# Kernel tuning notes

Measured on AMD Instinct MI355X. Metric: run time of the kernel, lower is better.

Reference implementation:

```python
import jax, jax.numpy as jnp
import numpy as np

N_NODES = 100000
HID = 128
N_LAYERS = 3
N_EDGES = 1600000
EPS = 1e-5


def setup_inputs() -> dict:
    key = jax.random.key(0)
    ks = jax.random.split(key, 10)
    H, L = HID, N_LAYERS
    # edge_index: row 0 = src, row 1 = dst (PyG source_to_target flow)
    edge_index = jax.random.randint(ks[0], (2, N_EDGES), 0, N_NODES, dtype=jnp.int32)
    # xavier-uniform embedding
    lim = float(np.sqrt(6.0 / (N_NODES + H)))
    emb = jax.random.uniform(ks[1], (N_NODES, H), jnp.float32, -lim, lim)
    s = 1.0 / np.sqrt(H)
    Wl = jax.random.uniform(ks[2], (L, H, H), jnp.float32, -s, s)  # lin_l (neighbors), has bias
    bl = jax.random.uniform(ks[3], (L, H), jnp.float32, -s, s)
    Wr = jax.random.uniform(ks[4], (L, H, H), jnp.float32, -s, s)  # lin_r (root), no bias
    ln_gamma = jnp.ones((L, H), jnp.float32)
    ln_beta = jnp.zeros((L, H), jnp.float32)
    sj = 1.0 / np.sqrt(H * (L + 1))
    jkW = jax.random.uniform(ks[5], (H, H * (L + 1)), jnp.float32, -sj, sj)
    jkb = jax.random.uniform(ks[6], (H,), jnp.float32, -sj, sj)
    return {"emb": emb, "Wl": Wl, "bl": bl, "Wr": Wr,
            "ln_gamma": ln_gamma, "ln_beta": ln_beta,
            "jkW": jkW, "jkb": jkb, "edge_index": edge_index}


def _layernorm(x, gamma, beta):
    mu = jnp.mean(x, axis=-1, keepdims=True)
    var = jnp.mean(jnp.square(x - mu), axis=-1, keepdims=True)
    return (x - mu) * jax.lax.rsqrt(var + EPS) * gamma + beta


def reference(emb, Wl, bl, Wr, ln_gamma, ln_beta, jkW, jkb, edge_index):
    src, dst = edge_index[0], edge_index[1]
    n = emb.shape[0]
    # in-degree for mean aggregation (clamped to avoid div-by-zero)
    deg = jax.ops.segment_sum(jnp.ones_like(dst, dtype=emb.dtype), dst, num_segments=n)
    inv_deg = (1.0 / jnp.maximum(deg, 1.0))[:, None]
    x = emb
    xs = [x]
    for i in range(N_LAYERS):
        x_prev = x
        # scatter-mean of neighbor features (gather [E,H] -> segment_sum [N,H])
        agg = jax.ops.segment_sum(x[src], dst, num_segments=n) * inv_deg
        # SAGEConv: lin_l(agg) + lin_r(x)
        x = agg @ Wl[i].T + bl[i] + x @ Wr[i].T
        x = _layernorm(x, ln_gamma[i], ln_beta[i])
        x = jax.nn.relu(x)
        # dropout is identity in eval mode
        if i > 0:
            x = x + x_prev
        xs.append(x)
    # jumping-knowledge concat + projection
    x = jnp.concatenate(xs, axis=1) @ jkW.T + jkb
    return x
```

## Files before the change

kernel.cpp:

```cpp
#include <hip/hip_runtime.h>
#include <hip/hip_bf16.h>
#include <stdint.h>

#define HID 128
#define BSHIFT 7
#define NBLK 64

typedef __attribute__((ext_vector_type(8))) __bf16 bf16x8;
typedef __attribute__((ext_vector_type(4))) float f32x4;

static __device__ __forceinline__ float bf2f(ushort h){
  union { uint u; float f; } c; c.u = ((uint)h) << 16; return c.f;
}
static __device__ __forceinline__ ushort f2bf(float f){
  union { float f; uint u; } c; c.f = f;
  uint u = c.u;
  return (ushort)((u + 0x7fffu + ((u >> 16) & 1u)) >> 16);
}
static __device__ __forceinline__ bf16x8 load8(const ushort* p){
  return *(const bf16x8*)p;
}

__global__ void k_cvt(const float* __restrict__ in, ushort* __restrict__ out, int n){
  int i = blockIdx.x * 256 + threadIdx.x;
  if (i < n) out[i] = f2bf(in[i]);
}

__global__ void k_cvtw(const float* __restrict__ Wl, const float* __restrict__ Wr,
                       ushort* __restrict__ outF, int total){
  int o = blockIdx.x * 256 + threadIdx.x;
  if (o >= total) return;
  int layer = o >> 15;
  int r = o & 32767;
  int e    = r & 7;
  int lane = (r >> 3) & 63;
  int jt   = (r >> 9) & 7;
  int mat  = (r >> 12) & 1;
  int kt   = r >> 13;
  int l16 = lane & 15, quad = lane >> 4;
  int j = l16 * 8 + jt;
  int k = kt * 32 + quad * 8 + e;
  const float* W = mat ? Wr : Wl;
  outF[o] = f2bf(W[layer * 16384 + j * 128 + k]);
}

__global__ void k_cvtjk(const float* __restrict__ jkW, ushort* __restrict__ outF){
  int o = blockIdx.x * 256 + threadIdx.x;
  int e    = o & 7;
  int lane = (o >> 3) & 63;
  int jt   = (o >> 9) & 7;
  int kt   = o >> 12;
  int l16 = lane & 15, quad = lane >> 4;
  int j = l16 * 4 + (jt & 3) + (jt >> 2) * 64;
  int k = kt * 32 + quad * 8 + e;
  outF[o] = f2bf(jkW[j * 512 + k]);
}

__global__ __launch_bounds__(1024) void k_count(
    const int* __restrict__ dst, int* __restrict__ rowcnt, int E, int NB, int es){
  __shared__ int h[1024];
  int blk = blockIdx.x;
  for (int i = threadIdx.x; i < NB; i += 1024) h[i] = 0;
  __syncthreads();
  int e0 = blk * es, e1 = min(e0 + es, E);
  for (int e = e0 + threadIdx.x; e < e1; e += 1024)
    atomicAdd(&h[dst[e] >> BSHIFT], 1);
  __syncthreads();
  for (int i = threadIdx.x; i < NB; i += 1024)
    rowcnt[blk * NB + i] = h[i];
}

__global__ __launch_bounds__(1024) void k_colscan(
    int* __restrict__ rowcnt, int* __restrict__ bbase, int NB, int nblk){
  int b = threadIdx.x;
  int total = 0;
  if (b < NB)
    for (int r = 0; r < nblk; r++) total += rowcnt[r * NB + b];
  int lane = b & 63, w = b >> 6;
  int x = total;
  #pragma unroll
  for (int d = 1; d < 64; d <<= 1){ int y = __shfl_up(x, d, 64); if (lane >= d) x += y; }
  __shared__ int tmp[16];
  if (lane == 63) tmp[w] = x;
  __syncthreads();
  if (b < 64){
    int s = (lane < 16) ? tmp[lane] : 0;
    #pragma unroll
    for (int d = 1; d < 16; d <<= 1){ int y = __shfl_up(s, d, 64); if (lane >= d) s += y; }
    if (lane < 16) tmp[lane] = s;
  }
  __syncthreads();
  int base = ((w > 0) ? tmp[w - 1] : 0) + x - total;
  if (b < NB){
    bbase[b] = base;
    int acc = base;
    for (int r = 0; r < nblk; r++){
      int v = rowcnt[r * NB + b];
      rowcnt[r * NB + b] = acc;
      acc += v;
    }
    if (b == NB - 1) bbase[NB] = acc;
  }
}

__global__ __launch_bounds__(1024) void k_place(
    const int* __restrict__ src, const int* __restrict__ dst,
    const int* __restrict__ rowcnt, uint* __restrict__ binned, int E, int NB, int es){
  __shared__ int cur[1024];
  int blk = blockIdx.x;
  for (int i = threadIdx.x; i < NB; i += 1024) cur[i] = rowcnt[blk * NB + i];
  __syncthreads();
  int e0 = blk * es, e1 = min(e0 + es, E);
  for (int e = e0 + threadIdx.x; e < e1; e += 1024){
    int d = dst[e];
    int b = d >> BSHIFT;
    int pos = atomicAdd(&cur[b], 1);
    binned[pos] = ((uint)src[e] << BSHIFT) | (uint)(d & 127);
  }
}

__global__ __launch_bounds__(256) void k_bpass(
    const uint* __restrict__ binned, const int* __restrict__ bbase,
    int* __restrict__ csr, int* __restrict__ offs, int* __restrict__ cnt, int N){
  int b = blockIdx.x;
  int n0 = b << BSHIFT;
  int tid = threadIdx.x;
  __shared__ int lcnt[128], loffs[128];
  if (tid < 128) lcnt[tid] = 0;
  __syncthreads();
  int base = bbase[b];
  int m = bbase[b + 1] - base;
  const uint* bp = binned + base;
  uint vv[12]; int slot[12];
  #pragma unroll
  for (int u = 0; u < 12; u++){
    int i = tid + u * 256;
    if (i < m){
      uint v = bp[i];
      vv[u] = v;
      slot[u] = atomicAdd(&lcnt[v & 127], 1);
    }
  }
  __syncthreads();
  if (tid < 64){
    int a0 = lcnt[tid * 2], a1 = lcnt[tid * 2 + 1];
    int s = a0 + a1;
    int x = s;
    #pragma unroll
    for (int d = 1; d < 64; d <<= 1){ int y = __shfl_up(x, d, 64); if (tid >= d) x += y; }
    int excl = x - s;
    loffs[tid * 2] = excl;
    loffs[tid * 2 + 1] = excl + a0;
  }
  __syncthreads();
  if (tid < 128 && n0 + tid < N){
    cnt[n0 + tid] = lcnt[tid];
    offs[n0 + tid] = base + loffs[tid];
  }
  #pragma unroll
  for (int u = 0; u < 12; u++){
    int i = tid + u * 256;
    if (i < m){
      uint v = vv[u];
      csr[base + loffs[v & 127] + slot[u]] = (int)(v >> BSHIFT);
    }
  }
}

__global__ __launch_bounds__(256) void k_aggregate(
    const ushort* __restrict__ x, const int* __restrict__ csr,
    const int* __restrict__ offs, const int* __restrict__ cnt,
    ushort* __restrict__ agg, int N){
  int node = blockIdx.x * 4 + (threadIdx.x >> 6);
  int lane = threadIdx.x & 63;
  if (node >= N) return;
  int half = lane >> 5;
  int l32  = lane & 31;
  int beg = offs[node], d = cnt[node];
  if (d == 0){
    if (half == 0){
      uint2 z = {0u, 0u};
      *(uint2*)(agg + (size_t)node * HID + l32 * 4) = z;
    }
    return;
  }
  const int* __restrict__ cp = csr + beg;
  float s0 = 0.f, s1 = 0.f, s2 = 0.f, s3 = 0.f;
  int i = 0;
  for (; i + 16 <= d; i += 16){
    int idx[8];
    #pragma unroll
    for (int u = 0; u < 8; u++) idx[u] = cp[i + 2 * u + half];
    uint2 v[8];
    #pragma unroll
    for (int u = 0; u < 8; u++)
      v[u] = *(const uint2*)(x + (size_t)idx[u] * HID + l32 * 4);
    #pragma unroll
    for (int u = 0; u < 8; u++){
      s0 += bf2f((ushort)v[u].x);
      s1 += bf2f((ushort)(v[u].x >> 16));
      s2 += bf2f((ushort)v[u].y);
      s3 += bf2f((ushort)(v[u].y >> 16));
    }
  }
  if (i < d){
    int idx[8]; float w[8];
    #pragma unroll
    for (int u = 0; u < 8; u++){
      int pos = i + 2 * u + half;
      bool ok = pos < d;
      pos = ok ? pos : d - 1;
      idx[u] = cp[pos];
      w[u] = ok ? 1.f : 0.f;
    }
    uint2 v[8];
    #pragma unroll
    for (int u = 0; u < 8; u++)
      v[u] = *(const uint2*)(x + (size_t)idx[u] * HID + l32 * 4);
    #pragma unroll
    for (int u = 0; u < 8; u++){
      s0 = fmaf(w[u], bf2f((ushort)v[u].x), s0);
      s1 = fmaf(w[u], bf2f((ushort)(v[u].x >> 16)), s1);
      s2 = fmaf(w[u], bf2f((ushort)v[u].y), s2);
      s3 = fmaf(w[u], bf2f((ushort)(v[u].y >> 16)), s3);
    }
  }
  s0 += __shfl_xor(s0, 32, 64);
  s1 += __shfl_xor(s1, 32, 64);
  s2 += __shfl_xor(s2, 32, 64);
  s3 += __shfl_xor(s3, 32, 64);
  if (half == 0){
    float inv = 1.0f / fmaxf((float)d, 1.0f);
    uint2 o;
    o.x = (uint)f2bf(s0 * inv) | ((uint)f2bf(s1 * inv) << 16);
    o.y = (uint)f2bf(s2 * inv) | ((uint)f2bf(s3 * inv) << 16);
    *(uint2*)(agg + (size_t)node * HID + l32 * 4) = o;
  }
}

template<int HAS_RES>
__global__ __launch_bounds__(256, 3) void k_layer(
    const ushort* __restrict__ agg, const ushort* __restrict__ xin,
    const ushort* __restrict__ Wf,
    const float* __restrict__ bl, const float* __restrict__ gamma,
    const float* __restrict__ beta,
    ushort* __restrict__ xout, int N){
  int tid = threadIdx.x;
  int wv = tid >> 6, lane = tid & 63;
  int quad = lane >> 4, l16 = lane & 15;
  int rowbase = blockIdx.x * 128 + wv * 32;
  int r0 = rowbase + l16;      if (r0 >= N) r0 = N - 1;
  int r1 = rowbase + 16 + l16; if (r1 >= N) r1 = N - 1;

  bf16x8 aL0[4], aL1[4], aR0[4], aR1[4];
  #pragma unroll
  for (int kt = 0; kt < 4; kt++){
    int ao = kt * 32 + quad * 8;
    aL0[kt] = load8(agg + (size_t)r0 * HID + ao);
    aL1[kt] = load8(agg + (size_t)r1 * HID + ao);
    aR0[kt] = load8(xin + (size_t)r0 * HID + ao);
    aR1[kt] = load8(xin + (size_t)r1 * HID + ao);
  }

  float4 bi0 = *(const float4*)(bl + l16 * 8);
  float4 bi1 = *(const float4*)(bl + l16 * 8 + 4);
  float4 g0 = *(const float4*)(gamma + l16 * 8);
  float4 g1 = *(const float4*)(gamma + l16 * 8 + 4);
  float4 be0 = *(const float4*)(beta + l16 * 8);
  float4 be1 = *(const float4*)(beta + l16 * 8 + 4);
  float gg[8] = {g0.x, g0.y, g0.z, g0.w, g1.x, g1.y, g1.z, g1.w};
  float bb[8] = {be0.x, be0.y, be0.z, be0.w, be1.x, be1.y, be1.z, be1.w};
  float bia[8] = {bi0.x, bi0.y, bi0.z, bi0.w, bi1.x, bi1.y, bi1.z, bi1.w};

  f32x4 acc[2][8];
  #pragma unroll
  for (int jt = 0; jt < 8; jt++){
    float b = bia[jt];
    f32x4 c = {b, b, b, b};
    acc[0][jt] = c; acc[1][jt] = c;
  }

  #pragma unroll
  for (int kt = 0; kt < 4; kt++){
    #pragma unroll
    for (int jt = 0; jt < 8; jt++){
      bf16x8 bL = load8(Wf + ((kt * 16 + jt) * 64 + lane) * 8);
      bf16x8 bR = load8(Wf + ((kt * 16 + 8 + jt) * 64 + lane) * 8);
      acc[0][jt] = __builtin_amdgcn_mfma_f32_16x16x32_bf16(aL0[kt], bL, acc[0][jt], 0, 0, 0);
      acc[1][jt] = __builtin_amdgcn_mfma_f32_16x16x32_bf16(aL1[kt], bL, acc[1][jt], 0, 0, 0);
      acc[0][jt] = __builtin_amdgcn_mfma_f32_16x16x32_bf16(aR0[kt], bR, acc[0][jt], 0, 0, 0);
      acc[1][jt] = __builtin_amdgcn_mfma_f32_16x16x32_bf16(aR1[kt], bR, acc[1][jt], 0, 0, 0);
    }
  }

  #pragma unroll
  for (int rt = 0; rt < 2; rt++){
    float s1[4] = {0,0,0,0}, s2[4] = {0,0,0,0};
    #pragma unroll
    for (int jt = 0; jt < 8; jt++){
      #pragma unroll
      for (int r = 0; r < 4; r++){ float v = acc[rt][jt][r]; s1[r] += v; s2[r] += v * v; }
    }
    #pragma unroll
    for (int m = 1; m < 16; m <<= 1){
      #pragma unroll
      for (int r = 0; r < 4; r++){
        s1[r] += __shfl_xor(s1[r], m, 64);
        s2[r] += __shfl_xor(s2[r], m, 64);
      }
    }
    #pragma unroll
    for (int r = 0; r < 4; r++){
      float mu = s1[r] * (1.f / 128.f);
      float var = s2[r] * (1.f / 128.f) - mu * mu;
      float rs = rsqrtf(var + 1e-5f);
      int row = rowbase + rt * 16 + quad * 4 + r;
      int rowc = row < N ? row : N - 1;
      uint rw[4] = {0u, 0u, 0u, 0u};
      if (HAS_RES){
        uint4 rv = *(const uint4*)(xin + (size_t)rowc * HID + l16 * 8);
        rw[0] = rv.x; rw[1] = rv.y; rw[2] = rv.z; rw[3] = rv.w;
      }
      uint ow[4];
      #pragma unroll
      for (int p = 0; p < 4; p++){
        float v0 = (acc[rt][2 * p][r] - mu) * rs * gg[2 * p] + bb[2 * p];
        float v1 = (acc[rt][2 * p + 1][r] - mu) * rs * gg[2 * p + 1] + bb[2 * p + 1];
        v0 = fmaxf(v0, 0.f);
        v1 = fmaxf(v1, 0.f);
        if (HAS_RES){
          v0 += bf2f((ushort)(rw[p] & 0xffffu));
          v1 += bf2f((ushort)(rw[p] >> 16));
        }
        ow[p] = (uint)f2bf(v0) | ((uint)f2bf(v1) << 16);
      }
      uint4 o;
      o.x = ow[0]; o.y = ow[1]; o.z = ow[2]; o.w = ow[3];
      if (row < N)
        *(uint4*)(xout + (size_t)row * HID + l16 * 8) = o;
    }
  }
}

__global__ __launch_bounds__(256, 3) void k_jk(
    const ushort* __restrict__ emb, const ushort* __restrict__ x1,
    const ushort* __restrict__ x2, const ushort* __restrict__ x3,
    const ushort* __restrict__ Wf,
    const float* __restrict__ jkb, float* __restrict__ out, int N){
  int tid = threadIdx.x;
  int wv = tid >> 6, lane = tid & 63;
  int quad = lane >> 4, l16 = lane & 15;
  int rowbase = blockIdx.x * 128 + wv * 32;
  int r0 = rowbase + l16;      if (r0 >= N) r0 = N - 1;
  int r1 = rowbase + 16 + l16; if (r1 >= N) r1 = N - 1;

  float4 jb0 = *(const float4*)(jkb + l16 * 4);
  float4 jb1 = *(const float4*)(jkb + 64 + l16 * 4);
  float bia[8] = {jb0.x, jb0.y, jb0.z, jb0.w, jb1.x, jb1.y, jb1.z, jb1.w};

  f32x4 acc[2][8];
  #pragma unroll
  for (int jt = 0; jt < 8; jt++){
    float b = bia[jt];
    f32x4 c = {b, b, b, b};
    acc[0][jt] = c; acc[1][jt] = c;
  }

  const ushort* srcs[4] = {emb, x1, x2, x3};
  #pragma unroll
  for (int s = 0; s < 4; s++){
    const ushort* sp = srcs[s];
    bf16x8 a0[4], a1[4];
    #pragma unroll
    for (int kt = 0; kt < 4; kt++){
      int ao = kt * 32 + quad * 8;
      a0[kt] = load8(sp + (size_t)r0 * HID + ao);
      a1[kt] = load8(sp + (size_t)r1 * HID + ao);
    }
    #pragma unroll
    for (int kt = 0; kt < 4; kt++){
      int ktg = s * 4 + kt;
      #pragma unroll
      for (int jt = 0; jt < 8; jt++){
        bf16x8 bW = load8(Wf + ((ktg * 8 + jt) * 64 + lane) * 8);
        acc[0][jt] = __builtin_amdgcn_mfma_f32_16x16x32_bf16(a0[kt], bW, acc[0][jt], 0, 0, 0);
        acc[1][jt] = __builtin_amdgcn_mfma_f32_16x16x32_bf16(a1[kt], bW, acc[1][jt], 0, 0, 0);
      }
    }
  }

  #pragma unroll
  for (int rt = 0; rt < 2; rt++){
    #pragma unroll
    for (int r = 0; r < 4; r++){
      int row = rowbase + rt * 16 + quad * 4 + r;
      if (row < N){
        f32x4 v0 = {acc[rt][0][r], acc[rt][1][r], acc[rt][2][r], acc[rt][3][r]};
        f32x4 v1 = {acc[rt][4][r], acc[rt][5][r], acc[rt][6][r], acc[rt][7][r]};
        *(f32x4*)(out + (size_t)row * HID + l16 * 4) = v0;
        *(f32x4*)(out + (size_t)row * HID + 64 + l16 * 4) = v1;
      }
    }
  }
}

extern "C" void kernel_launch(void* const* d_in, const int* in_sizes, int n_in,
                              void* d_out, int out_size, void* d_ws, size_t ws_size,
                              hipStream_t stream){
  const float* emb   = (const float*)d_in[0];
  const float* Wl    = (const float*)d_in[1];
  const float* bl    = (const float*)d_in[2];
  const float* Wr    = (const float*)d_in[3];
  const float* gamma = (const float*)d_in[4];
  const float* beta  = (const float*)d_in[5];
  const float* jkW   = (const float*)d_in[6];
  const float* jkb   = (const float*)d_in[7];
  const int*   eidx  = (const int*)d_in[8];
  int N = in_sizes[0] / HID;
  int E = in_sizes[8] / 2;
  const int* src = eidx;
  const int* dst = eidx + E;
  float* out = (float*)d_out;

  int NB = (N + 127) >> BSHIFT;
  int es = (E + NBLK - 1) / NBLK;

  char* w = (char*)d_ws;
  auto carve = [&](size_t bytes) -> char* {
    char* p = w; w += (bytes + 255) & ~(size_t)255; return p;
  };
  int Npad = ((N + 127) / 128) * 128;
  int* rowcnt   = (int*)carve((size_t)NBLK * NB * 4);
  int* bbase    = (int*)carve((size_t)(NB + 1) * 4);
  uint* binned  = (uint*)carve((size_t)E * 4);
  int* cnt      = (int*)carve((size_t)N * 4);
  int* offs     = (int*)carve((size_t)N * 4);
  int* csr      = (int*)carve((size_t)E * 4);
  ushort* Wfrag = (ushort*)carve((size_t)3 * 32768 * 2);
  ushort* jkWf  = (ushort*)carve((size_t)65536 * 2);
  ushort* embbf = (ushort*)carve((size_t)Npad * HID * 2);
  ushort* agg   = (ushort*)carve((size_t)Npad * HID * 2);
  ushort* x1    = (ushort*)carve((size_t)Npad * HID * 2);
  ushort* x2    = (ushort*)carve((size_t)Npad * HID * 2);
  ushort* x3    = (ushort*)carve((size_t)Npad * HID * 2);

  int nEmb = N * HID;
  k_cvtw<<<(3 * 32768 + 255) / 256, 256, 0, stream>>>(Wl, Wr, Wfrag, 3 * 32768);
  k_cvtjk<<<65536 / 256, 256, 0, stream>>>(jkW, jkWf);
  k_cvt<<<(nEmb + 255) / 256, 256, 0, stream>>>(emb, embbf, nEmb);

  k_count<<<NBLK, 1024, 0, stream>>>(dst, rowcnt, E, NB, es);
  k_colscan<<<1, 1024, 0, stream>>>(rowcnt, bbase, NB, NBLK);
  k_place<<<NBLK, 1024, 0, stream>>>(src, dst, rowcnt, binned, E, NB, es);
  k_bpass<<<NB, 256, 0, stream>>>(binned, bbase, csr, offs, cnt, N);

  int aggBlocks = (N + 3) / 4;
  int gemmBlocks = (N + 127) / 128;

  k_aggregate<<<aggBlocks, 256, 0, stream>>>(embbf, csr, offs, cnt, agg, N);
  k_layer<0><<<gemmBlocks, 256, 0, stream>>>(agg, embbf, Wfrag, bl, gamma, beta, x1, N);
  k_aggregate<<<aggBlocks, 256, 0, stream>>>(x1, csr, offs, cnt, agg, N);
  k_layer<1><<<gemmBlocks, 256, 0, stream>>>(agg, x1, Wfrag + 32768, bl + HID,
                                             gamma + HID, beta + HID, x2, N);
  k_aggregate<<<aggBlocks, 256, 0, stream>>>(x2, csr, offs, cnt, agg, N);
  k_layer<1><<<gemmBlocks, 256, 0, stream>>>(agg, x2, Wfrag + 2 * 32768, bl + 2 * HID,
                                             gamma + 2 * HID, beta + 2 * HID, x3, N);
  k_jk<<<gemmBlocks, 256, 0, stream>>>(embbf, x1, x2, x3, jkWf, jkb, out, N);
}
```

Measured before the change: 542.4 us.

## Cut register pressure in GEMM kernels and simplify gather address math

```diff
diff --git a/kernel.cpp b/kernel.cpp
--- a/kernel.cpp
+++ b/kernel.cpp
@@ -8,9 +8,13 @@
 
 typedef __attribute__((ext_vector_type(8))) __bf16 bf16x8;
 typedef __attribute__((ext_vector_type(4))) float f32x4;
+typedef __attribute__((ext_vector_type(2))) float f32x2;
 
 static __device__ __forceinline__ float bf2f(ushort h){
   union { uint u; float f; } c; c.u = ((uint)h) << 16; return c.f;
+}
+static __device__ __forceinline__ float u2f(uint u){
+  union { uint u; float f; } c; c.u = u; return c.f;
 }
 static __device__ __forceinline__ ushort f2bf(float f){
   union { float f; uint u; } c; c.f = f;
@@ -176,6 +180,7 @@
   if (node >= N) return;
   int half = lane >> 5;
   int l32  = lane & 31;
+  uint lb  = (uint)(l32 << 3);
   int beg = offs[node], d = cnt[node];
   if (d == 0){
     if (half == 0){
@@ -185,61 +190,61 @@
     return;
   }
   const int* __restrict__ cp = csr + beg;
-  float s0 = 0.f, s1 = 0.f, s2 = 0.f, s3 = 0.f;
+  const char* __restrict__ xb = (const char*)x;
+  f32x2 sx = {0.f, 0.f}, sy = {0.f, 0.f};
   int i = 0;
   for (; i + 16 <= d; i += 16){
-    int idx[8];
-    #pragma unroll
-    for (int u = 0; u < 8; u++) idx[u] = cp[i + 2 * u + half];
+    uint off[8];
+    #pragma unroll
+    for (int u = 0; u < 8; u++)
+      off[u] = ((uint)cp[i + 2 * u + half] << 8) + lb;
     uint2 v[8];
     #pragma unroll
     for (int u = 0; u < 8; u++)
-      v[u] = *(const uint2*)(x + (size_t)idx[u] * HID + l32 * 4);
+      v[u] = *(const uint2*)(xb + off[u]);
     #pragma unroll
     for (int u = 0; u < 8; u++){
-      s0 += bf2f((ushort)v[u].x);
-      s1 += bf2f((ushort)(v[u].x >> 16));
-      s2 += bf2f((ushort)v[u].y);
-      s3 += bf2f((ushort)(v[u].y >> 16));
+      f32x2 tx = { u2f(v[u].x << 16), u2f(v[u].x & 0xffff0000u) };
+      f32x2 ty = { u2f(v[u].y << 16), u2f(v[u].y & 0xffff0000u) };
+      sx += tx; sy += ty;
     }
   }
   if (i < d){
-    int idx[8]; float w[8];
+    uint off[8]; bool ok[8];
     #pragma unroll
     for (int u = 0; u < 8; u++){
       int pos = i + 2 * u + half;
-      bool ok = pos < d;
-      pos = ok ? pos : d - 1;
-      idx[u] = cp[pos];
-      w[u] = ok ? 1.f : 0.f;
+      ok[u] = pos < d;
+      off[u] = ((uint)cp[ok[u] ? pos : d - 1] << 8) + lb;
     }
     uint2 v[8];
     #pragma unroll
     for (int u = 0; u < 8; u++)
-      v[u] = *(const uint2*)(x + (size_t)idx[u] * HID + l32 * 4);
+      v[u] = *(const uint2*)(xb + off[u]);
     #pragma unroll
     for (int u = 0; u < 8; u++){
-      s0 = fmaf(w[u], bf2f((ushort)v[u].x), s0);
-      s1 = fmaf(w[u], bf2f((ushort)(v[u].x >> 16)), s1);
-      s2 = fmaf(w[u], bf2f((ushort)v[u].y), s2);
-      s3 = fmaf(w[u], bf2f((ushort)(v[u].y >> 16)), s3);
-    }
-  }
-  s0 += __shfl_xor(s0, 32, 64);
-  s1 += __shfl_xor(s1, 32, 64);
-  s2 += __shfl_xor(s2, 32, 64);
-  s3 += __shfl_xor(s3, 32, 64);
+      uint ax = ok[u] ? v[u].x : 0u;
+      uint ay = ok[u] ? v[u].y : 0u;
+      f32x2 tx = { u2f(ax << 16), u2f(ax & 0xffff0000u) };
+      f32x2 ty = { u2f(ay << 16), u2f(ay & 0xffff0000u) };
+      sx += tx; sy += ty;
+    }
+  }
+  sx.x += __shfl_xor(sx.x, 32, 64);
+  sx.y += __shfl_xor(sx.y, 32, 64);
+  sy.x += __shfl_xor(sy.x, 32, 64);
+  sy.y += __shfl_xor(sy.y, 32, 64);
   if (half == 0){
     float inv = 1.0f / fmaxf((float)d, 1.0f);
     uint2 o;
-    o.x = (uint)f2bf(s0 * inv) | ((uint)f2bf(s1 * inv) << 16);
-    o.y = (uint)f2bf(s2 * inv) | ((uint)f2bf(s3 * inv) << 16);
+    o.x = (uint)f2bf(sx.x * inv) | ((uint)f2bf(sx.y * inv) << 16);
+    o.y = (uint)f2bf(sy.x * inv) | ((uint)f2bf(sy.y * inv) << 16);
     *(uint2*)(agg + (size_t)node * HID + l32 * 4) = o;
   }
 }
 
 template<int HAS_RES>
-__global__ __launch_bounds__(256, 3) void k_layer(
+__global__ __launch_bounds__(256, 4) void k_layer(
     const ushort* __restrict__ agg, const ushort* __restrict__ xin,
     const ushort* __restrict__ Wf,
     const float* __restrict__ bl, const float* __restrict__ gamma,
@@ -251,47 +256,54 @@
   int rowbase = blockIdx.x * 128 + wv * 32;
   int r0 = rowbase + l16;      if (r0 >= N) r0 = N - 1;
   int r1 = rowbase + 16 + l16; if (r1 >= N) r1 = N - 1;
-
-  bf16x8 aL0[4], aL1[4], aR0[4], aR1[4];
+  int aq = quad * 8;
+
+  const ushort* pa0 = agg + (size_t)r0 * HID;
+  const ushort* pa1 = agg + (size_t)r1 * HID;
+  const ushort* px0 = xin + (size_t)r0 * HID;
+  const ushort* px1 = xin + (size_t)r1 * HID;
+
+  f32x4 acc[2][8];
+  {
+    float4 bi0 = *(const float4*)(bl + l16 * 8);
+    float4 bi1 = *(const float4*)(bl + l16 * 8 + 4);
+    float bia[8] = {bi0.x, bi0.y, bi0.z, bi0.w, bi1.x, bi1.y, bi1.z, bi1.w};
+    #pragma unroll
+    for (int jt = 0; jt < 8; jt++){
+      float b = bia[jt];
+      f32x4 c = {b, b, b, b};
+      acc[0][jt] = c; acc[1][jt] = c;
+    }
+  }
+
+  bf16x8 c0 = load8(pa0 + aq), c1 = load8(pa1 + aq);
+  bf16x8 c2 = load8(px0 + aq), c3 = load8(px1 + aq);
   #pragma unroll
   for (int kt = 0; kt < 4; kt++){
-    int ao = kt * 32 + quad * 8;
-    aL0[kt] = load8(agg + (size_t)r0 * HID + ao);
-    aL1[kt] = load8(agg + (size_t)r1 * HID + ao);
-    aR0[kt] = load8(xin + (size_t)r0 * HID + ao);
-    aR1[kt] = load8(xin + (size_t)r1 * HID + ao);
-  }
-
-  float4 bi0 = *(const float4*)(bl + l16 * 8);
-  float4 bi1 = *(const float4*)(bl + l16 * 8 + 4);
+    bf16x8 n0 = c0, n1 = c1, n2 = c2, n3 = c3;
+    if (kt < 3){
+      int ao = (kt + 1) * 32 + aq;
+      n0 = load8(pa0 + ao); n1 = load8(pa1 + ao);
+      n2 = load8(px0 + ao); n3 = load8(px1 + ao);
+    }
+    #pragma unroll
+    for (int jt = 0; jt < 8; jt++){
+      bf16x8 bL = load8(Wf + ((kt * 16 + jt) * 64 + lane) * 8);
+      bf16x8 bR = load8(Wf + ((kt * 16 + 8 + jt) * 64 + lane) * 8);
+      acc[0][jt] = __builtin_amdgcn_mfma_f32_16x16x32_bf16(c0, bL, acc[0][jt], 0, 0, 0);
+      acc[1][jt] = __builtin_amdgcn_mfma_f32_16x16x32_bf16(c1, bL, acc[1][jt], 0, 0, 0);
+      acc[0][jt] = __builtin_amdgcn_mfma_f32_16x16x32_bf16(c2, bR, acc[0][jt], 0, 0, 0);
+      acc[1][jt] = __builtin_amdgcn_mfma_f32_16x16x32_bf16(c3, bR, acc[1][jt], 0, 0, 0);
+    }
+    c0 = n0; c1 = n1; c2 = n2; c3 = n3;
+  }
+
   float4 g0 = *(const float4*)(gamma + l16 * 8);
   float4 g1 = *(const float4*)(gamma + l16 * 8 + 4);
   float4 be0 = *(const float4*)(beta + l16 * 8);
   float4 be1 = *(const float4*)(beta + l16 * 8 + 4);
   float gg[8] = {g0.x, g0.y, g0.z, g0.w, g1.x, g1.y, g1.z, g1.w};
   float bb[8] = {be0.x, be0.y, be0.z, be0.w, be1.x, be1.y, be1.z, be1.w};
-  float bia[8] = {bi0.x, bi0.y, bi0.z, bi0.w, bi1.x, bi1.y, bi1.z, bi1.w};
-
-  f32x4 acc[2][8];
-  #pragma unroll
-  for (int jt = 0; jt < 8; jt++){
-    float b = bia[jt];
-    f32x4 c = {b, b, b, b};
-    acc[0][jt] = c; acc[1][jt] = c;
-  }
-
-  #pragma unroll
-  for (int kt = 0; kt < 4; kt++){
-    #pragma unroll
-    for (int jt = 0; jt < 8; jt++){
-      bf16x8 bL = load8(Wf + ((kt * 16 + jt) * 64 + lane) * 8);
-      bf16x8 bR = load8(Wf + ((kt * 16 + 8 + jt) * 64 + lane) * 8);
-      acc[0][jt] = __builtin_amdgcn_mfma_f32_16x16x32_bf16(aL0[kt], bL, acc[0][jt], 0, 0, 0);
-      acc[1][jt] = __builtin_amdgcn_mfma_f32_16x16x32_bf16(aL1[kt], bL, acc[1][jt], 0, 0, 0);
-      acc[0][jt] = __builtin_amdgcn_mfma_f32_16x16x32_bf16(aR0[kt], bR, acc[0][jt], 0, 0, 0);
-      acc[1][jt] = __builtin_amdgcn_mfma_f32_16x16x32_bf16(aR1[kt], bR, acc[1][jt], 0, 0, 0);
-    }
-  }
 
   #pragma unroll
   for (int rt = 0; rt < 2; rt++){
@@ -342,7 +354,7 @@
   }
 }
 
-__global__ __launch_bounds__(256, 3) void k_jk(
+__global__ __launch_bounds__(256, 4) void k_jk(
     const ushort* __restrict__ emb, const ushort* __restrict__ x1,
     const ushort* __restrict__ x2, const ushort* __restrict__ x3,
     const ushort* __restrict__ Wf,
@@ -353,50 +365,51 @@
   int rowbase = blockIdx.x * 128 + wv * 32;
   int r0 = rowbase + l16;      if (r0 >= N) r0 = N - 1;
   int r1 = rowbase + 16 + l16; if (r1 >= N) r1 = N - 1;
+  int aq = quad * 8;
+  size_t o0 = (size_t)r0 * HID, o1 = (size_t)r1 * HID;
+
+  f32x4 acc[2][8];
+  #pragma unroll
+  for (int jt = 0; jt < 8; jt++){
+    f32x4 z = {0.f, 0.f, 0.f, 0.f};
+    acc[0][jt] = z; acc[1][jt] = z;
+  }
+
+  const ushort* srcs[4] = {emb, x1, x2, x3};
+  bf16x8 a0 = load8(emb + o0 + aq);
+  bf16x8 a1 = load8(emb + o1 + aq);
+  #pragma unroll
+  for (int ktg = 0; ktg < 16; ktg++){
+    bf16x8 n0 = a0, n1 = a1;
+    if (ktg < 15){
+      const ushort* sp = srcs[(ktg + 1) >> 2];
+      int ao = ((ktg + 1) & 3) * 32 + aq;
+      n0 = load8(sp + o0 + ao);
+      n1 = load8(sp + o1 + ao);
+    }
+    #pragma unroll
+    for (int jt = 0; jt < 8; jt++){
+      bf16x8 bW = load8(Wf + ((ktg * 8 + jt) * 64 + lane) * 8);
+      acc[0][jt] = __builtin_amdgcn_mfma_f32_16x16x32_bf16(a0, bW, acc[0][jt], 0, 0, 0);
+      acc[1][jt] = __builtin_amdgcn_mfma_f32_16x16x32_bf16(a1, bW, acc[1][jt], 0, 0, 0);
+    }
+    a0 = n0; a1 = n1;
+  }
 
   float4 jb0 = *(const float4*)(jkb + l16 * 4);
   float4 jb1 = *(const float4*)(jkb + 64 + l16 * 4);
   float bia[8] = {jb0.x, jb0.y, jb0.z, jb0.w, jb1.x, jb1.y, jb1.z, jb1.w};
 
-  f32x4 acc[2][8];
-  #pragma unroll
-  for (int jt = 0; jt < 8; jt++){
-    float b = bia[jt];
-    f32x4 c = {b, b, b, b};
-    acc[0][jt] = c; acc[1][jt] = c;
-  }
-
-  const ushort* srcs[4] = {emb, x1, x2, x3};
-  #pragma unroll
-  for (int s = 0; s < 4; s++){
-    const ushort* sp = srcs[s];
-    bf16x8 a0[4], a1[4];
-    #pragma unroll
-    for (int kt = 0; kt < 4; kt++){
-      int ao = kt * 32 + quad * 8;
-      a0[kt] = load8(sp + (size_t)r0 * HID + ao);
-      a1[kt] = load8(sp + (size_t)r1 * HID + ao);
-    }
-    #pragma unroll
-    for (int kt = 0; kt < 4; kt++){
-      int ktg = s * 4 + kt;
-      #pragma unroll
-      for (int jt = 0; jt < 8; jt++){
-        bf16x8 bW = load8(Wf + ((ktg * 8 + jt) * 64 + lane) * 8);
-        acc[0][jt] = __builtin_amdgcn_mfma_f32_16x16x32_bf16(a0[kt], bW, acc[0][jt], 0, 0, 0);
-        acc[1][jt] = __builtin_amdgcn_mfma_f32_16x16x32_bf16(a1[kt], bW, acc[1][jt], 0, 0, 0);
-      }
-    }
-  }
-
   #pragma unroll
   for (int rt = 0; rt < 2; rt++){
     #pragma unroll
     for (int r = 0; r < 4; r++){
       int row = rowbase + rt * 16 + quad * 4 + r;
       if (row < N){
-        f32x4 v0 = {acc[rt][0][r], acc[rt][1][r], acc[rt][2][r], acc[rt][3][r]};
-        f32x4 v1 = {acc[rt][4][r], acc[rt][5][r], acc[rt][6][r], acc[rt][7][r]};
+        f32x4 v0 = {acc[rt][0][r] + bia[0], acc[rt][1][r] + bia[1],
+                    acc[rt][2][r] + bia[2], acc[rt][3][r] + bia[3]};
+        f32x4 v1 = {acc[rt][4][r] + bia[4], acc[rt][5][r] + bia[5],
+                    acc[rt][6][r] + bia[6], acc[rt][7][r] + bia[7]};
         *(f32x4*)(out + (size_t)row * HID + l16 * 4) = v0;
         *(f32x4*)(out + (size_t)row * HID + 64 + l16 * 4) = v1;
       }
```

Result: faster. 519.2 us (-4.3%).
